# Optimization experiments

Measured on AMD Instinct MI355X. Metric: run time of the kernel, lower is better.

The kernel has to match this reference:

```python
import jax, jax.numpy as jnp
import numpy as np

NUM_CLASSES = 81
THRESHOLD = 0.5
NEGPOS_RATIO = 3
VARIANCE = (0.1, 0.2)


def point_form(p):
    # center-size -> corner form
    return jnp.concatenate([p[:, :2] - p[:, 2:] / 2, p[:, :2] + p[:, 2:] / 2], axis=1)


def jaccard(box_a, box_b):
    # box_a: [O,4] corners, box_b: [P,4] corners -> IoU [O,P]
    lt = jnp.maximum(box_a[:, None, :2], box_b[None, :, :2])
    rb = jnp.minimum(box_a[:, None, 2:], box_b[None, :, 2:])
    wh = jnp.clip(rb - lt, 0.0)
    inter = wh[..., 0] * wh[..., 1]
    area_a = ((box_a[:, 2] - box_a[:, 0]) * (box_a[:, 3] - box_a[:, 1]))[:, None]
    area_b = ((box_b[:, 2] - box_b[:, 0]) * (box_b[:, 3] - box_b[:, 1]))[None, :]
    return inter / (area_a + area_b - inter)


def encode(matched, priors, variances):
    # matched: [P,4] corner GT, priors: [P,4] center-size
    g_cxcy = (matched[:, :2] + matched[:, 2:]) / 2 - priors[:, :2]
    g_cxcy = g_cxcy / (variances[0] * priors[:, 2:])
    g_wh = (matched[:, 2:] - matched[:, :2]) / priors[:, 2:]
    g_wh = jnp.log(g_wh) / variances[1]
    return jnp.concatenate([g_cxcy, g_wh], axis=1)


def match_one(truths, labels, priors):
    overlaps = jaccard(truths, point_form(priors))   # [O,P]
    best_prior_idx = jnp.argmax(overlaps, axis=1)     # [O] best prior per truth
    best_truth_overlap = jnp.max(overlaps, axis=0)    # [P]
    best_truth_idx = jnp.argmax(overlaps, axis=0)     # [P] best truth per prior
    # force each truth's best prior to match that truth
    best_truth_overlap = best_truth_overlap.at[best_prior_idx].set(2.0)
    best_truth_idx = best_truth_idx.at[best_prior_idx].set(jnp.arange(truths.shape[0]))
    matched = truths[best_truth_idx]                  # [P,4]
    conf = labels[best_truth_idx].astype(jnp.int32) + 1
    conf = jnp.where(best_truth_overlap < THRESHOLD, 0, conf)
    loc = encode(matched, priors, VARIANCE)
    return loc, conf


def _loss(loc_data, conf_data, targets, priors):
    B, P, C = conf_data.shape
    loc_t, conf_t = jax.vmap(lambda t: match_one(t[:, :4], t[:, 4], priors))(targets)
    pos = conf_t > 0                                  # [B,P]
    # smooth-L1 (beta=1) over positive priors, sum reduction
    d = loc_data - loc_t
    sl1 = jnp.where(jnp.abs(d) < 1.0, 0.5 * d * d, jnp.abs(d) - 0.5)
    loss_l = jnp.sum(jnp.where(pos[..., None], sl1, 0.0))
    # per-prior CE used both for mining ranking and the final conf loss
    ce = jax.nn.logsumexp(conf_data, axis=-1) - jnp.take_along_axis(
        conf_data, conf_t[..., None], axis=-1)[..., 0]   # [B,P]
    # hard negative mining: zero positives, double argsort for rank
    loss_c_rank = jnp.where(pos, 0.0, ce)
    loss_idx = jnp.argsort(-loss_c_rank, axis=1)
    idx_rank = jnp.argsort(loss_idx, axis=1)
    num_pos = jnp.sum(pos, axis=1, keepdims=True)     # [B,1]
    num_neg = jnp.minimum(NEGPOS_RATIO * num_pos, P - 1)
    neg = idx_rank < num_neg
    sel = pos | neg
    loss_c = jnp.sum(jnp.where(sel, ce, 0.0))
    N = jnp.sum(num_pos).astype(loc_data.dtype)
    return loss_l / N, loss_c / N


def setup_inputs():
    key = jax.random.key(0)
    kl, kc, kb1, kb2, kll, kp1, kp2 = jax.random.split(key, 7)
    B, P, O, C = 64, 8732, 50, NUM_CLASSES
    loc_data = jax.random.normal(kl, (B, P, 4), jnp.float32)
    conf_data = jax.random.normal(kc, (B, P, C), jnp.float32)
    # valid GT boxes in corner form inside [0,1]
    cxcy = jax.random.uniform(kb1, (B, O, 2), minval=0.2, maxval=0.8)
    wh = jax.random.uniform(kb2, (B, O, 2), minval=0.05, maxval=0.3)
    boxes = jnp.concatenate([cxcy - wh / 2, cxcy + wh / 2], axis=-1)
    labels = jax.random.randint(kll, (B, O), 0, C - 1).astype(jnp.float32)
    targets = jnp.concatenate([boxes, labels[..., None]], axis=-1)  # [B,O,5]
    # priors in center-size form
    pcxcy = jax.random.uniform(kp1, (P, 2), minval=0.05, maxval=0.95)
    pwh = jax.random.uniform(kp2, (P, 2), minval=0.05, maxval=0.5)
    priors = jnp.concatenate([pcxcy, pwh], axis=-1)
    return {"loc_data": loc_data, "conf_data": conf_data, "targets": targets, "priors": priors}


def reference(loc_data, conf_data, targets, priors):
    return _loss(loc_data, conf_data, targets, priors)
```

## Files before the change

### kernel.cpp

```cpp
#include <hip/hip_runtime.h>
#include <float.h>

#pragma clang fp contract(off)

typedef unsigned long long ull;
typedef unsigned int u32;

#define THRESH 0.5f
#define PPT 4
#define SEL_T 512
#define ENC_SEG 1024


__device__ __forceinline__ float sl1(float d) {
    float a = fabsf(d);
    return (a < 1.f) ? 0.5f * d * d : a - 0.5f;
}

__global__ __launch_bounds__(256) void k_prep(
        const float* __restrict__ targets, const float* __restrict__ priors,
        const float* __restrict__ conf,
        float* __restrict__ bto, int* __restrict__ bti, ull* __restrict__ tbest,
        float* __restrict__ lse,
        u32* __restrict__ zws, int nz,
        int P, int O, int S, int SB, int SPEC, int G, int npairs, long long BP) {
    const int bid = blockIdx.x;
    __shared__ float4 tbox[128];
    __shared__ float tarea[128];
    if (bid == 0)
        for (int i = threadIdx.x; i < nz; i += 256) zws[i] = 0;

    long long t0 = (long long)bid * SPEC;
    int k0 = (int)(t0 / G);
    bool is_spec = (int)((t0 + SPEC) / G) > k0;

    if (!is_spec) {
        int lb = bid - k0;
        long long r = (long long)lb * 256 + threadIdx.x;
        if (r < BP) {
            const float* rp = conf + r * 81;
            float s0 = 0.f, s1 = 0.f;
#pragma unroll
            for (int k = 0; k < 10; k++) {
                float4 v = *(const float4*)(rp + 4 * k);
                s0 += __expf(v.x); s0 += __expf(v.y);
                s0 += __expf(v.z); s0 += __expf(v.w);
            }
            s0 += __expf(rp[40]);
#pragma unroll
            for (int k = 0; k < 10; k++) {
                float4 v = *(const float4*)(rp + 41 + 4 * k);
                s1 += __expf(v.x); s1 += __expf(v.y);
                s1 += __expf(v.z); s1 += __expf(v.w);
            }
            lse[r] = __logf(s0 + s1);
        }
        return;
    }

    const int sidx = k0;
    if (sidx < SB) {
        const int b = sidx / S, seg = sidx % S;
        const float* trow = targets + (size_t)b * O * 5;
        for (int o = threadIdx.x; o < O; o += 256) {
            float x1 = trow[o * 5 + 0], y1 = trow[o * 5 + 1];
            float x2 = trow[o * 5 + 2], y2 = trow[o * 5 + 3];
            tbox[o] = make_float4(x1, y1, x2, y2);
            tarea[o] = (x2 - x1) * (y2 - y1);
        }
        __syncthreads();
        const int p0 = seg * (256 * PPT);
        float px1[PPT], py1[PPT], px2[PPT], py2[PPT], pa[PPT];
        float bestv[PPT]; int besto[PPT]; int pidx[PPT];
#pragma unroll
        for (int j = 0; j < PPT; j++) {
            int p = p0 + (int)threadIdx.x + j * 256;
            pidx[j] = p; bestv[j] = -1.f; besto[j] = 0;
            if (p < P) {
                float4 pr = ((const float4*)priors)[p];
                px1[j] = pr.x - pr.z / 2.f;
                py1[j] = pr.y - pr.w / 2.f;
                px2[j] = pr.x + pr.z / 2.f;
                py2[j] = pr.y + pr.w / 2.f;
                pa[j] = (px2[j] - px1[j]) * (py2[j] - py1[j]);
            } else {
                px1[j] = 2.f; py1[j] = 2.f; px2[j] = 2.f; py2[j] = 2.f; pa[j] = 1.f;
            }
        }
        for (int o = 0; o < O; o++) {
            float4 t = tbox[o];
            float ta = tarea[o];
#pragma unroll
            for (int j = 0; j < PPT; j++) {
                float lx = fmaxf(t.x, px1[j]), ly = fmaxf(t.y, py1[j]);
                float rx = fminf(t.z, px2[j]), ry = fminf(t.w, py2[j]);
                float wx = fmaxf(rx - lx, 0.f), wy = fmaxf(ry - ly, 0.f);
                float inter = wx * wy;
                float iou = 0.f;
                if (inter > 0.f) iou = inter / (ta + pa[j] - inter);
                if (iou > bestv[j]) { bestv[j] = iou; besto[j] = o; }
            }
        }
#pragma unroll
        for (int j = 0; j < PPT; j++) {
            if (pidx[j] < P) {
                bto[(size_t)b * P + pidx[j]] = bestv[j];
                bti[(size_t)b * P + pidx[j]] = besto[j];
            }
        }
    } else {
        int g = (sidx - SB) * 4 + ((int)threadIdx.x >> 6);
        int lane = threadIdx.x & 63;
        if (g >= npairs) return;
        int OP = (O + 1) >> 1;
        int b = g / OP;
        int o0 = (g % OP) * 2;
        const float* trow = targets + ((size_t)b * O + o0) * 5;
        float ax1 = trow[0], ay1 = trow[1], ax2 = trow[2], ay2 = trow[3];
        float ta0 = (ax2 - ax1) * (ay2 - ay1);
        bool has1 = (o0 + 1) < O;
        float cx1 = 0, cy1 = 0, cx2 = 0, cy2 = 0, ta1 = 1.f;
        if (has1) {
            cx1 = trow[5]; cy1 = trow[6]; cx2 = trow[7]; cy2 = trow[8];
            ta1 = (cx2 - cx1) * (cy2 - cy1);
        }
        ull k0v = 0, k1v = 0;
        for (int p = lane; p < P; p += 64) {
            float4 pr = ((const float4*)priors)[p];
            float bx1 = pr.x - pr.z / 2.f;
            float by1 = pr.y - pr.w / 2.f;
            float bx2 = pr.x + pr.z / 2.f;
            float by2 = pr.y + pr.w / 2.f;
            float pa = (bx2 - bx1) * (by2 - by1);
            u32 np = ~(u32)p;
            {
                float lx = fmaxf(ax1, bx1), ly = fmaxf(ay1, by1);
                float rx = fminf(ax2, bx2), ry = fminf(ay2, by2);
                float wx = fmaxf(rx - lx, 0.f), wy = fmaxf(ry - ly, 0.f);
                float inter = wx * wy;
                float iou = 0.f;
                if (inter > 0.f) iou = inter / (ta0 + pa - inter);
                ull key = ((ull)__float_as_uint(iou) << 32) | np;
                if (key > k0v) k0v = key;
            }
            if (has1) {
                float lx = fmaxf(cx1, bx1), ly = fmaxf(cy1, by1);
                float rx = fminf(cx2, bx2), ry = fminf(cy2, by2);
                float wx = fmaxf(rx - lx, 0.f), wy = fmaxf(ry - ly, 0.f);
                float inter = wx * wy;
                float iou = 0.f;
                if (inter > 0.f) iou = inter / (ta1 + pa - inter);
                ull key = ((ull)__float_as_uint(iou) << 32) | np;
                if (key > k1v) k1v = key;
            }
        }
        for (int off = 32; off; off >>= 1) {
            ull a = __shfl_xor(k0v, off); if (a > k0v) k0v = a;
            ull d = __shfl_xor(k1v, off); if (d > k1v) k1v = d;
        }
        if (lane == 0) {
            tbest[(size_t)b * O + o0] = k0v;
            if (has1) tbest[(size_t)b * O + o0 + 1] = k1v;
        }
    }
}

__global__ __launch_bounds__(256) void k_encode_ce(
        const float* __restrict__ targets, const float* __restrict__ priors,
        const float* __restrict__ loc_data, const float* __restrict__ conf,
        const ull* __restrict__ tbest, const float* __restrict__ lse,
        float* __restrict__ F,
        int* __restrict__ conf_t,
        int* __restrict__ num_pos, float* __restrict__ loss_l,
        int P, int O) {
    const int b = blockIdx.y, seg = blockIdx.x;
    __shared__ float tr[64 * 5];
    __shared__ int ov[ENC_SEG];
    __shared__ float redf[4]; __shared__ int redi[4];
    const int p0 = seg * ENC_SEG;
    const int p1 = min(p0 + ENC_SEG, P);
    const int nprior = p1 - p0;
    const float* trow = targets + (size_t)b * O * 5;
    for (int i = threadIdx.x; i < O * 5; i += 256) tr[i] = trow[i];
    for (int i = threadIdx.x; i < nprior; i += 256) ov[i] = -1;
    __syncthreads();
    if ((int)threadIdx.x < O) {
        ull tb = tbest[(size_t)b * O + threadIdx.x];
        u32 p = ~(u32)(tb & 0xFFFFFFFFULL);
        if (p >= (u32)P) p = 0;
        if ((int)p >= p0 && (int)p < p1) atomicMax(&ov[p - p0], (int)threadIdx.x);
    }
    __syncthreads();
    float ll = 0.f; int cnt = 0;
    for (int p = p0 + (int)threadIdx.x; p < p1; p += 256) {
        size_t idx = (size_t)b * P + p;
        int o = conf_t[idx];
        int ovv = ov[p - p0];
        bool forced = ovv >= 0;
        if (forced) o = ovv;
        float ovl = F[idx];
        int cv = (!forced && ovl < THRESH) ? 0 : ((int)tr[o * 5 + 4] + 1);
        conf_t[idx] = cv;
        if (cv > 0) {
            cnt++;
            float4 pr = ((const float4*)priors)[p];
            float mx1 = tr[o * 5], my1 = tr[o * 5 + 1];
            float mx2 = tr[o * 5 + 2], my2 = tr[o * 5 + 3];
            float gx = ((mx1 + mx2) / 2.f - pr.x) / (0.1f * pr.z);
            float gy = ((my1 + my2) / 2.f - pr.y) / (0.1f * pr.w);
            float gw = logf((mx2 - mx1) / pr.z) / 0.2f;
            float gh = logf((my2 - my1) / pr.w) / 0.2f;
            float4 ld = ((const float4*)loc_data)[idx];
            ll += sl1(ld.x - gx) + sl1(ld.y - gy) + sl1(ld.z - gw) + sl1(ld.w - gh);
        }
        float tv = conf[idx * 81 + cv];
        F[idx] = lse[idx] - tv;
    }
    for (int off = 32; off; off >>= 1) {
        ll += __shfl_down(ll, off);
        cnt += __shfl_down(cnt, off);
    }
    int w = threadIdx.x >> 6;
    if ((threadIdx.x & 63) == 0) { redf[w] = ll; redi[w] = cnt; }
    __syncthreads();
    if (threadIdx.x == 0) {
        float l = 0; int c = 0;
        for (int i = 0; i < 4; i++) { l += redf[i]; c += redi[i]; }
        if (c) atomicAdd(&num_pos[b], c);
        atomicAdd(&loss_l[b], l);
    }
}

__global__ __launch_bounds__(SEL_T) void k_select(
        const float* __restrict__ ce, const int* __restrict__ conf_t,
        const int* __restrict__ num_pos, const float* __restrict__ loss_l,
        float* __restrict__ acc, u32* __restrict__ ticket,
        float* __restrict__ out, int P, int B) {
    extern __shared__ u32 sk[];
    __shared__ u32 whist[SEL_T / 64][16];
    __shared__ u32 hist[16];
    __shared__ float redf[SEL_T / 64]; __shared__ u32 redu[SEL_T / 64];
    __shared__ u32 sh_pval; __shared__ int sh_rem;
    const int b = blockIdx.x;
    const size_t base = (size_t)b * P;
    const int lane = threadIdx.x & 63;
    const int w = threadIdx.x >> 6;
    const int NW = SEL_T / 64;

    float ps = 0.f;
    for (int p = threadIdx.x; p < P; p += SEL_T) {
        int c = conf_t[base + p];
        float v = ce[base + p];
        u32 key;
        if (c > 0) { ps += v; key = 0u; }
        else key = __float_as_uint(fmaxf(v, 0.f));
        sk[p] = key;
    }
    for (int off = 32; off; off >>= 1) ps += __shfl_down(ps, off);
    if (lane == 0) redf[w] = ps;
    __syncthreads();
    float pos_sum = 0.f;
    if (threadIdx.x == 0) {
        for (int i = 0; i < NW; i++) pos_sum += redf[i];
    }

    const int np = num_pos[b];
    const int k = min(3 * np, P - 1);
    u32 pval = 0, pmask = 0; int rem = k;
    if (k > 0) {
        for (int shift = 28; shift >= 0; shift -= 4) {
            __syncthreads();
            ull a0 = 0, a1 = 0;
            for (int p = threadIdx.x; p < P; p += SEL_T) {
                u32 key = sk[p];
                if ((key & pmask) == pval) {
                    u32 dig = (key >> shift) & 15u;
                    ull inc = 1ull << ((dig & 7u) * 8u);
                    if (dig < 8u) a0 += inc; else a1 += inc;
                }
            }
            const ull M = 0x00FF00FF00FF00FFull;
            ull e0 = a0 & M, e1 = (a0 >> 8) & M, e2 = a1 & M, e3 = (a1 >> 8) & M;
            for (int off = 32; off; off >>= 1) {
                e0 += __shfl_xor(e0, off);
                e1 += __shfl_xor(e1, off);
                e2 += __shfl_xor(e2, off);
                e3 += __shfl_xor(e3, off);
            }
            if (lane == 0) {
#pragma unroll
                for (int j = 0; j < 4; j++) {
                    whist[w][2 * j]     = (u32)((e0 >> (16 * j)) & 0xFFFF);
                    whist[w][2 * j + 1] = (u32)((e1 >> (16 * j)) & 0xFFFF);
                    whist[w][8 + 2 * j]     = (u32)((e2 >> (16 * j)) & 0xFFFF);
                    whist[w][8 + 2 * j + 1] = (u32)((e3 >> (16 * j)) & 0xFFFF);
                }
            }
            __syncthreads();
            if (threadIdx.x < 16) {
                u32 h = 0;
                for (int i = 0; i < NW; i++) h += whist[i][threadIdx.x];
                hist[threadIdx.x] = h;
            }
            __syncthreads();
            if (threadIdx.x == 0) {
                u32 accu = 0; int d = 15;
                for (; d > 0; d--) {
                    u32 h = hist[d];
                    if (accu + h >= (u32)rem) break;
                    accu += h;
                }
                sh_pval = pval | ((u32)d << shift);
                sh_rem = rem - (int)accu;
            }
            __syncthreads();
            pval = sh_pval; rem = sh_rem; pmask |= (0xFu << shift);
        }
    }

    float sgt = 0.f; u32 cgt = 0;
    if (k > 0) {
        for (int p = threadIdx.x; p < P; p += SEL_T) {
            u32 key = sk[p];
            if (key > pval) { sgt += __uint_as_float(key); cgt++; }
        }
    }
    for (int off = 32; off; off >>= 1) {
        sgt += __shfl_down(sgt, off);
        cgt += __shfl_down(cgt, off);
    }
    __syncthreads();
    if (lane == 0) { redf[w] = sgt; redu[w] = cgt; }
    __syncthreads();
    if (threadIdx.x == 0) {
        float s = 0.f; u32 c = 0;
        for (int i = 0; i < NW; i++) { s += redf[i]; c += redu[i]; }
        float t = __uint_as_float(pval);
        float lc_b = pos_sum + ((k > 0) ? (s + (float)(k - (int)c) * t) : 0.f);
        atomicAdd(&acc[0], (float)np);
        atomicAdd(&acc[1], loss_l[b]);
        atomicAdd(&acc[2], lc_b);
        __threadfence();
        u32 tk = atomicAdd(ticket, 1u);
        if (tk == (u32)(B - 1)) {
            float n  = atomicAdd(&acc[0], 0.f);
            float ll = atomicAdd(&acc[1], 0.f);
            float lc = atomicAdd(&acc[2], 0.f);
            out[0] = ll / n;
            out[1] = lc / n;
        }
    }
}


extern "C" void kernel_launch(void* const* d_in, const int* in_sizes, int n_in,
                              void* d_out, int out_size, void* d_ws, size_t ws_size,
                              hipStream_t stream) {
    const float* loc     = (const float*)d_in[0];
    const float* conf    = (const float*)d_in[1];
    const float* targets = (const float*)d_in[2];
    const float* priors  = (const float*)d_in[3];

    const int P = in_sizes[3] / 4;
    const int B = in_sizes[0] / (P * 4);
    const int O = in_sizes[2] / (B * 5);
    const long long BP = (long long)B * P;

    char* ws = (char*)d_ws;
    size_t off = 0;
    int*   num_pos = (int*)(ws + off);   off += (size_t)B * sizeof(int);
    float* loss_l  = (float*)(ws + off); off += (size_t)B * sizeof(float);
    float* acc     = (float*)(ws + off); off += 4 * sizeof(float);
    u32*   ticket  = (u32*)(ws + off);   off += sizeof(u32);
    const int zwords = (int)(off >> 2);
    off = (off + 7) & ~(size_t)7;
    ull*   tbest   = (ull*)(ws + off);   off += (size_t)B * O * sizeof(ull);
    float* F       = (float*)(ws + off); off += (size_t)BP * sizeof(float);
    int*   I       = (int*)(ws + off);   off += (size_t)BP * sizeof(int);
    float* L       = (float*)(ws + off); off += (size_t)BP * sizeof(float);

    const int SEG = 256 * PPT;
    const int S = (P + SEG - 1) / SEG;
    const int SB = S * B;
    const int npairs = B * ((O + 1) / 2);
    const int TB = (npairs + 3) / 4;
    const int CB = (int)((BP + 255) / 256);
    const int SPEC = SB + TB;
    const int G = CB + SPEC;
    k_prep<<<G, 256, 0, stream>>>(targets, priors, conf, F, I, tbest, L,
                                  (u32*)ws, zwords, P, O, S, SB, SPEC, G, npairs, BP);

    const int S2 = (P + ENC_SEG - 1) / ENC_SEG;
    k_encode_ce<<<dim3(S2, B), 256, 0, stream>>>(targets, priors, loc, conf, tbest, L,
                                                 F, I, num_pos, loss_l, P, O);

    k_select<<<B, SEL_T, (size_t)P * sizeof(u32), stream>>>(F, I, num_pos, loss_l,
                                                            acc, ticket, (float*)d_out, P, B);
}
```

Before: 368.4 us.

## Split log-sum-exp into its own kernel using coalesced global-to-LDS staging

Moves the per-row log-sum-exp over the conf tensor out of the fused prep kernel into a dedicated kernel. Each block stages 128 rows of 81 floats into LDS with global_load_lds so the loads are fully coalesced, then two threads per row compute the sum. This replaces strided per-thread float4 reads of 324-byte rows. The IoU matching work becomes a separate launch, which adds launch overhead and loses the interleaving of the two workloads inside one grid.

Measured after the change: 373.4 us. About the same (+1.4%).

```diff
diff --git a/kernel.cpp b/kernel.cpp
--- a/kernel.cpp
+++ b/kernel.cpp
@@ -10,6 +10,7 @@
 #define PPT 4
 #define SEL_T 512
 #define ENC_SEG 1024
+#define LSE_ROWS 128
 
 
 __device__ __forceinline__ float sl1(float d) {
@@ -17,50 +18,66 @@
     return (a < 1.f) ? 0.5f * d * d : a - 0.5f;
 }
 
-__global__ __launch_bounds__(256) void k_prep(
+__device__ __forceinline__ void gload16(const void* g, void* l) {
+    __builtin_amdgcn_global_load_lds(
+        (const __attribute__((address_space(1))) void*)g,
+        (__attribute__((address_space(3))) void*)l, 16, 0, 0);
+}
+__device__ __forceinline__ void gload4(const void* g, void* l) {
+    __builtin_amdgcn_global_load_lds(
+        (const __attribute__((address_space(1))) void*)g,
+        (__attribute__((address_space(3))) void*)l, 4, 0, 0);
+}
+
+__global__ __launch_bounds__(256) void k_lse(
+        const float* __restrict__ conf, float* __restrict__ lse,
+        u32* __restrict__ zws, int nz, long long BP) {
+    __shared__ float s[LSE_ROWS * 81];
+    const int bid = blockIdx.x;
+    if (bid == 0)
+        for (int i = threadIdx.x; i < nz; i += 256) zws[i] = 0;
+    const long long r0 = (long long)bid * LSE_ROWS;
+    const int w = threadIdx.x >> 6;
+    const int lane = threadIdx.x & 63;
+    const char* gbase = (const char*)(conf + r0 * 81);
+
+    if (r0 + LSE_ROWS <= BP) {
+        for (int i = w * 10; i < w * 10 + 10; i++)
+            gload16(gbase + (size_t)i * 1024 + lane * 16, (char*)s + i * 1024);
+        if (w == 0) {
+            gload4(gbase + 40960 + lane * 4, (char*)s + 40960);
+            gload4(gbase + 41216 + lane * 4, (char*)s + 41216);
+        }
+        asm volatile("s_waitcnt vmcnt(0)" ::: "memory");
+    } else {
+        int nfl = (int)(BP - r0) * 81;
+        const float* src = (const float*)gbase;
+        for (int i = threadIdx.x; i < nfl; i += 256) s[i] = src[i];
+    }
+    __syncthreads();
+
+    const int row = threadIdx.x >> 1;
+    const int half = threadIdx.x & 1;
+    if (r0 + row < BP) {
+        const float* rp = s + row * 81;
+        const int c0 = half * 41;
+        const int cn = half ? 40 : 41;
+        float sum = 0.f;
+        for (int j = 0; j < cn; j++) sum += __expf(rp[c0 + j]);
+        sum += __shfl_xor(sum, 1);
+        if (half == 0) lse[r0 + row] = __logf(sum);
+    }
+}
+
+__global__ __launch_bounds__(256) void k_spec(
         const float* __restrict__ targets, const float* __restrict__ priors,
-        const float* __restrict__ conf,
         float* __restrict__ bto, int* __restrict__ bti, ull* __restrict__ tbest,
-        float* __restrict__ lse,
-        u32* __restrict__ zws, int nz,
-        int P, int O, int S, int SB, int SPEC, int G, int npairs, long long BP) {
+        int P, int O, int S, int SB, int npairs) {
     const int bid = blockIdx.x;
     __shared__ float4 tbox[128];
     __shared__ float tarea[128];
-    if (bid == 0)
-        for (int i = threadIdx.x; i < nz; i += 256) zws[i] = 0;
-
-    long long t0 = (long long)bid * SPEC;
-    int k0 = (int)(t0 / G);
-    bool is_spec = (int)((t0 + SPEC) / G) > k0;
-
-    if (!is_spec) {
-        int lb = bid - k0;
-        long long r = (long long)lb * 256 + threadIdx.x;
-        if (r < BP) {
-            const float* rp = conf + r * 81;
-            float s0 = 0.f, s1 = 0.f;
-#pragma unroll
-            for (int k = 0; k < 10; k++) {
-                float4 v = *(const float4*)(rp + 4 * k);
-                s0 += __expf(v.x); s0 += __expf(v.y);
-                s0 += __expf(v.z); s0 += __expf(v.w);
-            }
-            s0 += __expf(rp[40]);
-#pragma unroll
-            for (int k = 0; k < 10; k++) {
-                float4 v = *(const float4*)(rp + 41 + 4 * k);
-                s1 += __expf(v.x); s1 += __expf(v.y);
-                s1 += __expf(v.z); s1 += __expf(v.w);
-            }
-            lse[r] = __logf(s0 + s1);
-        }
-        return;
-    }
-
-    const int sidx = k0;
-    if (sidx < SB) {
-        const int b = sidx / S, seg = sidx % S;
+    if (bid < SB) {
+        const int b = bid / S, seg = bid % S;
         const float* trow = targets + (size_t)b * O * 5;
         for (int o = threadIdx.x; o < O; o += 256) {
             float x1 = trow[o * 5 + 0], y1 = trow[o * 5 + 1];
@@ -109,7 +126,7 @@
             }
         }
     } else {
-        int g = (sidx - SB) * 4 + ((int)threadIdx.x >> 6);
+        int g = (bid - SB) * 4 + ((int)threadIdx.x >> 6);
         int lane = threadIdx.x & 63;
         if (g >= npairs) return;
         int OP = (O + 1) >> 1;
@@ -379,16 +396,15 @@
     int*   I       = (int*)(ws + off);   off += (size_t)BP * sizeof(int);
     float* L       = (float*)(ws + off); off += (size_t)BP * sizeof(float);
 
+    const int CB = (int)((BP + LSE_ROWS - 1) / LSE_ROWS);
+    k_lse<<<CB, 256, 0, stream>>>(conf, L, (u32*)ws, zwords, BP);
+
     const int SEG = 256 * PPT;
     const int S = (P + SEG - 1) / SEG;
     const int SB = S * B;
     const int npairs = B * ((O + 1) / 2);
     const int TB = (npairs + 3) / 4;
-    const int CB = (int)((BP + 255) / 256);
-    const int SPEC = SB + TB;
-    const int G = CB + SPEC;
-    k_prep<<<G, 256, 0, stream>>>(targets, priors, conf, F, I, tbest, L,
-                                  (u32*)ws, zwords, P, O, S, SB, SPEC, G, npairs, BP);
+    k_spec<<<SB + TB, 256, 0, stream>>>(targets, priors, F, I, tbest, P, O, S, SB, npairs);
 
     const int S2 = (P + ENC_SEG - 1) / ENC_SEG;
     k_encode_ce<<<dim3(S2, B), 256, 0, stream>>>(targets, priors, loc, conf, tbest, L,
```
